# Performance work log

Hardware: AMD Instinct MI355X
Metric: run time of the kernel (lower is better)

Reference implementation:

```python
import jax, jax.numpy as jnp
from jax import lax
import numpy as np

N, E = 10000, 120000
IN_DIM = 128
HID = 32        # hidden_dim
HEADS = 8
OUT = 32        # out_dim
HD = HID * HEADS  # 256
EPS = 1e-5


def _bn(x, g, b):
    # BatchNorm1d (training-mode batch stats, deterministic reference)
    mu = x.mean(0)
    var = x.var(0)
    return g * (x - mu) * lax.rsqrt(var + EPS) + b


def _seg_softmax(logits, seg, n):
    # softmax over edges grouped by destination node, per head
    m = jax.ops.segment_max(logits, seg, num_segments=n)
    ex = jnp.exp(logits - m[seg])
    s = jax.ops.segment_sum(ex, seg, num_segments=n)
    return ex / (s[seg] + 1e-16)


def _gat_layer(h, src, dst, fc_w, a_l, a_r, bn_g, bn_b, heads, out, residual):
    n = h.shape[0]
    h_in = h
    feat = (h @ fc_w).reshape(n, heads, out)      # [N,H,D]
    el = (feat * a_l).sum(-1)                     # [N,H]
    er = (feat * a_r).sum(-1)
    logits = jax.nn.leaky_relu(el[src] + er[dst], 0.2)  # [E,H]
    alpha = _seg_softmax(logits, dst, n)
    rst = jax.ops.segment_sum(alpha[..., None] * feat[src], dst, num_segments=n)
    rst = rst.reshape(n, heads * out)
    rst = _bn(rst, bn_g, bn_b)
    rst = jax.nn.elu(rst)
    if residual:
        rst = h_in + rst
    return rst


def setup_inputs():
    key = jax.random.key(0)
    ks = jax.random.split(key, 20)
    s = 0.02
    d = {}
    d["h"] = jax.random.normal(ks[0], (N, IN_DIM), jnp.float32)
    d["e"] = jax.random.normal(ks[1], (E, IN_DIM), jnp.float32)
    d["src"] = jax.random.randint(ks[2], (E,), 0, N, jnp.int32)
    d["dst"] = jax.random.randint(ks[3], (E,), 0, N, jnp.int32)
    d["W_emb"] = jax.random.normal(ks[4], (IN_DIM, HD)) * s
    d["b_emb"] = jnp.zeros((HD,))
    d["W_p1"] = jax.random.normal(ks[5], (IN_DIM, HID * HID)) * s
    d["b_p1"] = jnp.zeros((HID * HID,))
    d["W_p2"] = jax.random.normal(ks[6], (IN_DIM, HID)) * s
    d["b_p2"] = jnp.zeros((HID,))
    d["W_conv"] = jax.random.normal(ks[7], (1, 2, 3)) * s  # Conv1d(2->1,k=3)
    d["b_conv"] = jnp.zeros((1,))
    d["W_ep2"] = jax.random.normal(ks[8], (IN_DIM, HD)) * s
    d["b_ep2"] = jnp.zeros((HD,))
    d["W_ep3"] = jax.random.normal(ks[9], (HID, HD)) * s
    d["b_ep3"] = jnp.zeros((HD,))
    d["bn_g"] = jnp.ones((HD,))
    d["bn_b"] = jnp.zeros((HD,))
    d["fc1"] = jax.random.normal(ks[10], (HD, HD)) * s
    d["al1"] = jax.random.normal(ks[11], (HEADS, HID)) * s
    d["ar1"] = jax.random.normal(ks[12], (HEADS, HID)) * s
    d["g1"] = jnp.ones((HD,))
    d["b1"] = jnp.zeros((HD,))
    d["fc2"] = jax.random.normal(ks[13], (HD, OUT)) * s
    d["al2"] = jax.random.normal(ks[14], (1, OUT)) * s
    d["ar2"] = jax.random.normal(ks[15], (1, OUT)) * s
    d["g2"] = jnp.ones((OUT,))
    d["b2"] = jnp.zeros((OUT,))
    return d


def reference(h, e, src, dst, W_emb, b_emb, W_p1, b_p1, W_p2, b_p2,
              W_conv, b_conv, W_ep2, b_ep2, W_ep3, b_ep3, bn_g, bn_b,
              fc1, al1, ar1, g1, b1, fc2, al2, ar2, g2, b2):
    # local edge feature: Conv1d over stacked (src,dst) node feats
    edge = jnp.stack([h[src], h[dst]], axis=1)  # [E,2,IN_DIM]
    conv = lax.conv_general_dilated(edge, W_conv, (1,), [(1, 1)],
                                    dimension_numbers=("NCH", "OIH", "NCH"))
    lr_local = conv[:, 0, :] + b_conv[0]         # [E,IN_DIM]
    lr_e_local = lr_local @ W_ep2 + b_ep2        # [E,HD]
    # low-rank global affinity: mm[i,j,k] = sum_d p1[i,k,d]*p2[j,d],
    # gathered only at edges (same math as the dense NxNxHID tensor)
    p1 = (h @ W_p1 + b_p1).reshape(-1, HID, HID)  # [N,HID,HID]
    p2 = h @ W_p2 + b_p2                          # [N,HID]
    lr_glob = jnp.einsum("ekd,ed->ek", p1[src], p2[dst])  # [E,HID]
    lr_e_global = lr_glob @ W_ep3 + b_ep3        # [E,HD]
    e_feat = jax.nn.relu(_bn(lr_e_local + lr_e_global, bn_g, bn_b))
    del e_feat  # default 'dgl' GATLayer ignores e; kept for faithfulness of math
    hh = h @ W_emb + b_emb                       # embedding_h
    hh = _gat_layer(hh, src, dst, fc1, al1, ar1, g1, b1, HEADS, HID, True)
    hh = _gat_layer(hh, src, dst, fc2, al2, ar2, g2, b2, 1, OUT, False)
    return hh
```

## Files before the change

### kernel.cpp

```cpp
#include <hip/hip_runtime.h>
#include <hip/hip_bf16.h>
#include <math.h>


#define HDIM 256
#define NHEADS 8
#define ODIM 32

typedef unsigned short u16;
typedef __attribute__((ext_vector_type(8))) short short8;
typedef __attribute__((ext_vector_type(4))) float f32x4;

__device__ __forceinline__ float bf2f(u16 u) { return __uint_as_float(((unsigned)u) << 16); }
__device__ __forceinline__ u16 f2bf(float f) {
    unsigned x = __float_as_uint(f);
    return (u16)((x + 0x7FFFu + ((x >> 16) & 1u)) >> 16);
}

__global__ __launch_bounds__(256) void prep_kernel(const float* __restrict__ in_h, const float* __restrict__ W_emb,
                                                   const float* __restrict__ fc1, const float* __restrict__ fc2,
                                                   u16* __restrict__ Ah, u16* __restrict__ Bemb,
                                                   u16* __restrict__ Bfc1, u16* __restrict__ Bfc2, int n4) {
    int job = blockIdx.y;
    int idx = blockIdx.x * 256 + threadIdx.x;
    if (job == 0) {
        if (idx >= n4) return;
        float4 v = ((const float4*)in_h)[idx];
        ushort4 o = {f2bf(v.x), f2bf(v.y), f2bf(v.z), f2bf(v.w)};
        ((ushort4*)Ah)[idx] = o;
        return;
    }
    const float* B;
    u16* O;
    int K, NC;
    if (job == 1) { B = W_emb; O = Bemb; K = 128; NC = 256; }
    else if (job == 2) { B = fc1; O = Bfc1; K = 256; NC = 256; }
    else { B = fc2; O = Bfc2; K = 256; NC = 32; }
    int KB = K / 32;
    int TOT = (NC / 16) * KB * 64;
    if (idx >= TOT) return;
    int lane = idx & 63;
    int kb = (idx >> 6) % KB;
    int ct = (idx >> 6) / KB;
    int n = ct * 16 + (lane & 15);
    int k0 = kb * 32 + (lane >> 4) * 8;
    u16* dst = O + (size_t)idx * 8;
#pragma unroll
    for (int j = 0; j < 8; j++) dst[j] = f2bf(B[(size_t)(k0 + j) * NC + n]);
}

__global__ __launch_bounds__(256) void deg_kernel(const int* __restrict__ dst, int* __restrict__ deg, int E, int N) {
    int i = blockIdx.x * 256 + threadIdx.x;
    if (i < E) {
        unsigned d = (unsigned)dst[i];
        if (d < (unsigned)N) atomicAdd(&deg[d], 1);
    }
}

__global__ __launch_bounds__(256) void scan_kernel(const int* __restrict__ deg, int* __restrict__ offs,
                                                   int* __restrict__ cursor, int n) {
    __shared__ int part[256];
    int t = threadIdx.x;
    int chunk = (n + 255) / 256;
    int lo = t * chunk, hi = lo + chunk;
    if (hi > n) hi = n;
    if (lo > n) lo = n;
    int s = 0;
    for (int i = lo; i < hi; i++) s += deg[i];
    part[t] = s;
    __syncthreads();
    if (t == 0) {
        int run = 0;
        for (int j = 0; j < 256; j++) { int v = part[j]; part[j] = run; run += v; }
        offs[n] = run;
    }
    __syncthreads();
    int run = part[t];
    for (int i = lo; i < hi; i++) {
        offs[i] = run;
        cursor[i] = run;
        run += deg[i];
    }
}

__global__ __launch_bounds__(256) void fill_kernel(const int* __restrict__ src, const int* __restrict__ dst,
                                                   int* __restrict__ cursor, int* __restrict__ srcs, int E, int N) {
    int i = blockIdx.x * 256 + threadIdx.x;
    if (i < E) {
        unsigned d = (unsigned)dst[i];
        if (d < (unsigned)N) {
            int p = atomicAdd(&cursor[d], 1);
            if ((unsigned)p < (unsigned)E) srcs[p] = src[i];
        }
    }
}

template <int K, int NC, bool BIAS, typename OutT>
__global__ __launch_bounds__(256) void gemm_mfma(const u16* __restrict__ A, const u16* __restrict__ Bsw,
                                                 const float* __restrict__ bias, OutT* __restrict__ C, int M) {
    constexpr int KB = K / 32;
    constexpr int NCT = NC / 16;
    const int lane = threadIdx.x & 63;
    const int r0 = blockIdx.x * 64 + (threadIdx.x >> 6) * 16;
    if (r0 >= M) return;
    const int m = lane & 15, q = lane >> 4;
    const int row = r0 + m;
    short8 a[KB];
#pragma unroll
    for (int kb = 0; kb < KB; kb++) {
        if (row < M) a[kb] = *(const short8*)(A + (size_t)row * K + kb * 32 + q * 8);
        else a[kb] = (short8){0, 0, 0, 0, 0, 0, 0, 0};
    }
    const short8* B8 = (const short8*)Bsw;
#pragma unroll 1
    for (int ct = 0; ct < NCT; ct++) {
        f32x4 acc = {0.f, 0.f, 0.f, 0.f};
#pragma unroll
        for (int kb = 0; kb < KB; kb++)
            acc = __builtin_amdgcn_mfma_f32_16x16x32_bf16(a[kb], B8[(ct * KB + kb) * 64 + lane], acc, 0, 0, 0);
        float bv = BIAS ? bias[ct * 16 + m] : 0.f;
#pragma unroll
        for (int r = 0; r < 4; r++) {
            int ro = r0 + q * 4 + r;
            if (ro < M) {
                float v = acc[r] + bv;
                if constexpr (sizeof(OutT) == 2) C[(size_t)ro * NC + ct * 16 + m] = f2bf(v);
                else C[(size_t)ro * NC + ct * 16 + m] = v;
            }
        }
    }
}

__global__ __launch_bounds__(256) void gemm_fc1_elr(const u16* __restrict__ A, const u16* __restrict__ Bsw,
                                                    const float* __restrict__ al, const float* __restrict__ ar,
                                                    u16* __restrict__ featC, u16* __restrict__ el,
                                                    u16* __restrict__ er, int M) {
    __shared__ u16 tile[64][256];
    const int lane = threadIdx.x & 63;
    const int wq = threadIdx.x >> 6;
    const int rb = blockIdx.x * 64;
    const int r0 = rb + wq * 16;
    const int m = lane & 15, q = lane >> 4;
    const int row = r0 + m;
    short8 a[8];
#pragma unroll
    for (int kb = 0; kb < 8; kb++) {
        if (row < M) a[kb] = *(const short8*)(A + (size_t)row * 256 + kb * 32 + q * 8);
        else a[kb] = (short8){0, 0, 0, 0, 0, 0, 0, 0};
    }
    const short8* B8 = (const short8*)Bsw;
#pragma unroll 1
    for (int ct = 0; ct < 16; ct++) {
        f32x4 acc = {0.f, 0.f, 0.f, 0.f};
#pragma unroll
        for (int kb = 0; kb < 8; kb++)
            acc = __builtin_amdgcn_mfma_f32_16x16x32_bf16(a[kb], B8[(ct * 8 + kb) * 64 + lane], acc, 0, 0, 0);
#pragma unroll
        for (int r = 0; r < 4; r++) {
            int rl = wq * 16 + q * 4 + r;
            int ro = rb + rl;
            u16 v = 0;
            if (ro < M) {
                v = f2bf(acc[r]);
                featC[(size_t)ro * 256 + ct * 16 + m] = v;
            }
            tile[rl][ct * 16 + m] = v;
        }
    }
    __syncthreads();
    int t = threadIdx.x;
#pragma unroll
    for (int task = t; task < 512; task += 256) {
        int nl = task >> 3, h = task & 7;
        int node = rb + nl;
        if (node >= M) continue;
        float a_ = 0.f, b_ = 0.f;
#pragma unroll
        for (int d = 0; d < 32; d++) {
            float fv = bf2f(tile[nl][h * 32 + d]);
            a_ += fv * al[h * 32 + d];
            b_ += fv * ar[h * 32 + d];
        }
        el[node * 8 + h] = f2bf(a_);
        er[node * 8 + h] = f2bf(b_);
    }
}

__device__ __forceinline__ float edgew(float l) {
    l = (l > 0.f) ? l : 0.2f * l;
    l = fminf(fmaxf(l, -30.f), 30.f);
    return __expf(l);
}

__global__ __launch_bounds__(256) void agg1_fused(const u16* __restrict__ feat, const u16* __restrict__ el,
                                                  const u16* __restrict__ er, const int* __restrict__ offs,
                                                  const int* __restrict__ srcs, u16* __restrict__ rst, int N, int E) {
    const int node = blockIdx.x * 4 + (threadIdx.x >> 6);
    const int lane = threadIdx.x & 63;
    if (node >= N) return;
    const int h = lane >> 3;
    int beg = offs[node], end = offs[node + 1];
    if (beg < 0) beg = 0;
    if (end > E) end = E;
    float ern = bf2f(er[node * 8 + h]);
    float ax = 0.f, ay = 0.f, az = 0.f, aw = 0.f, sw = 0.f;
    int j = beg;
    int end4 = beg + ((end - beg) & ~3);
    for (; j < end4; j += 4) {
        int s0 = srcs[j], s1 = srcs[j + 1], s2 = srcs[j + 2], s3 = srcs[j + 3];
        unsigned c0 = (unsigned)s0 < (unsigned)N, c1 = (unsigned)s1 < (unsigned)N;
        unsigned c2 = (unsigned)s2 < (unsigned)N, c3 = (unsigned)s3 < (unsigned)N;
        s0 = c0 ? s0 : 0; s1 = c1 ? s1 : 0; s2 = c2 ? s2 : 0; s3 = c3 ? s3 : 0;
        u16 e0 = el[s0 * 8 + h], e1 = el[s1 * 8 + h], e2 = el[s2 * 8 + h], e3 = el[s3 * 8 + h];
        ushort4 f0 = *(const ushort4*)(feat + (size_t)s0 * 256 + lane * 4);
        ushort4 f1 = *(const ushort4*)(feat + (size_t)s1 * 256 + lane * 4);
        ushort4 f2 = *(const ushort4*)(feat + (size_t)s2 * 256 + lane * 4);
        ushort4 f3 = *(const ushort4*)(feat + (size_t)s3 * 256 + lane * 4);
        float w0 = c0 ? edgew(bf2f(e0) + ern) : 0.f;
        float w1 = c1 ? edgew(bf2f(e1) + ern) : 0.f;
        float w2 = c2 ? edgew(bf2f(e2) + ern) : 0.f;
        float w3 = c3 ? edgew(bf2f(e3) + ern) : 0.f;
        sw += w0 + w1 + w2 + w3;
        ax += w0 * bf2f(f0.x) + w1 * bf2f(f1.x) + w2 * bf2f(f2.x) + w3 * bf2f(f3.x);
        ay += w0 * bf2f(f0.y) + w1 * bf2f(f1.y) + w2 * bf2f(f2.y) + w3 * bf2f(f3.y);
        az += w0 * bf2f(f0.z) + w1 * bf2f(f1.z) + w2 * bf2f(f2.z) + w3 * bf2f(f3.z);
        aw += w0 * bf2f(f0.w) + w1 * bf2f(f1.w) + w2 * bf2f(f2.w) + w3 * bf2f(f3.w);
    }
    for (; j < end; j++) {
        int s = srcs[j];
        if ((unsigned)s >= (unsigned)N) continue;
        float wv = edgew(bf2f(el[s * 8 + h]) + ern);
        ushort4 f4 = *(const ushort4*)(feat + (size_t)s * 256 + lane * 4);
        sw += wv;
        ax += wv * bf2f(f4.x);
        ay += wv * bf2f(f4.y);
        az += wv * bf2f(f4.z);
        aw += wv * bf2f(f4.w);
    }
    float inv = 1.f / (sw + 1e-16f);
    ushort4 o;
    o.x = f2bf(ax * inv); o.y = f2bf(ay * inv); o.z = f2bf(az * inv); o.w = f2bf(aw * inv);
    *(ushort4*)(rst + (size_t)node * 256 + lane * 4) = o;
}

__global__ __launch_bounds__(256) void bn_stats256(const u16* __restrict__ X, float* __restrict__ stats,
                                                   int rows, int RPB) {
    int t = threadIdx.x;
    int rbeg = blockIdx.x * RPB;
    int rend = rbeg + RPB;
    if (rend > rows) rend = rows;
    float s = 0.f, s2 = 0.f;
    for (int r = rbeg; r < rend; r++) {
        float x = bf2f(X[(long)r * 256 + t]);
        s += x;
        s2 += x * x;
    }
    atomicAdd(&stats[t], s);
    atomicAdd(&stats[256 + t], s2);
}

__global__ __launch_bounds__(256) void bn_stats32(const float* __restrict__ X, float* __restrict__ stats,
                                                  int rows, int RPB) {
    __shared__ float ss[256], ss2[256];
    int t = threadIdx.x, c = t & 31, rs = t >> 5;
    int rbeg = blockIdx.x * RPB;
    int rend = rbeg + RPB;
    if (rend > rows) rend = rows;
    float s = 0.f, s2 = 0.f;
    for (int r = rbeg + rs; r < rend; r += 8) {
        float x = X[(long)r * 32 + c];
        s += x;
        s2 += x * x;
    }
    ss[t] = s;
    ss2[t] = s2;
    __syncthreads();
    if (t < 32) {
        for (int j = 32; j < 256; j += 32) { s += ss[t + j]; s2 += ss2[t + j]; }
        atomicAdd(&stats[c], s);
        atomicAdd(&stats[32 + c], s2);
    }
}

__global__ __launch_bounds__(256) void gemm_fc2_fused(const u16* __restrict__ rst, const u16* __restrict__ hh,
                                                      const float* __restrict__ stats, const float* __restrict__ g,
                                                      const float* __restrict__ b, const u16* __restrict__ Bsw,
                                                      const float* __restrict__ al2, const float* __restrict__ ar2,
                                                      float* __restrict__ feat2, float* __restrict__ el2,
                                                      float* __restrict__ er2, int M, float invN) {
    __shared__ float sc[256], sh[256];
    __shared__ float tile[64][32];
    const int t = threadIdx.x;
    {
        float mu = stats[t] * invN;
        float var = fmaxf(stats[256 + t] * invN - mu * mu, 0.f);
        float s = g[t] * rsqrtf(var + 1e-5f);
        sc[t] = s;
        sh[t] = b[t] - mu * s;
    }
    __syncthreads();
    const int lane = t & 63, wq = t >> 6;
    const int rb = blockIdx.x * 64;
    const int m = lane & 15, q = lane >> 4;
    const int row = rb + wq * 16 + m;
    short8 a[8];
#pragma unroll
    for (int kb = 0; kb < 8; kb++) {
        if (row < M) {
            int k0 = kb * 32 + q * 8;
            ushort4 r01 = *(const ushort4*)(rst + (size_t)row * 256 + k0);
            ushort4 r23 = *(const ushort4*)(rst + (size_t)row * 256 + k0 + 4);
            ushort4 h01 = *(const ushort4*)(hh + (size_t)row * 256 + k0);
            ushort4 h23 = *(const ushort4*)(hh + (size_t)row * 256 + k0 + 4);
            u16 rv[8] = {r01.x, r01.y, r01.z, r01.w, r23.x, r23.y, r23.z, r23.w};
            u16 hv[8] = {h01.x, h01.y, h01.z, h01.w, h23.x, h23.y, h23.z, h23.w};
            short8 av;
#pragma unroll
            for (int j = 0; j < 8; j++) {
                int c = k0 + j;
                float y = sc[c] * bf2f(rv[j]) + sh[c];
                y = (y > 0.f) ? y : expm1f(y);
                av[j] = (short)f2bf(bf2f(hv[j]) + y);
            }
            a[kb] = av;
        } else a[kb] = (short8){0, 0, 0, 0, 0, 0, 0, 0};
    }
    const short8* B8 = (const short8*)Bsw;
#pragma unroll
    for (int ct = 0; ct < 2; ct++) {
        f32x4 acc = {0.f, 0.f, 0.f, 0.f};
#pragma unroll
        for (int kb = 0; kb < 8; kb++)
            acc = __builtin_amdgcn_mfma_f32_16x16x32_bf16(a[kb], B8[(ct * 8 + kb) * 64 + lane], acc, 0, 0, 0);
#pragma unroll
        for (int r = 0; r < 4; r++) {
            int rl = wq * 16 + q * 4 + r;
            int ro = rb + rl;
            float v = 0.f;
            if (ro < M) {
                v = acc[r];
                feat2[(size_t)ro * 32 + ct * 16 + m] = v;
            }
            tile[rl][ct * 16 + m] = v;
        }
    }
    __syncthreads();
    if (t < 64) {
        int node = rb + t;
        if (node < M) {
            float a_ = 0.f, b_ = 0.f;
#pragma unroll
            for (int d = 0; d < 32; d++) {
                float fv = tile[t][d];
                a_ += fv * al2[d];
                b_ += fv * ar2[d];
            }
            el2[node] = a_;
            er2[node] = b_;
        }
    }
}

__global__ __launch_bounds__(256) void agg2_fused(const float* __restrict__ feat, const float* __restrict__ el,
                                                  const float* __restrict__ er, const int* __restrict__ offs,
                                                  const int* __restrict__ srcs, float* __restrict__ rst,
                                                  int N, int E) {
    const int t = threadIdx.x;
    const int node = blockIdx.x * 8 + (t >> 5);
    const int d = t & 31;
    if (node >= N) return;
    int beg = offs[node], end = offs[node + 1];
    if (beg < 0) beg = 0;
    if (end > E) end = E;
    float ern = er[node];
    float acc = 0.f, sw = 0.f;
#pragma unroll 2
    for (int j = beg; j < end; j++) {
        int s = srcs[j];
        if ((unsigned)s >= (unsigned)N) continue;
        float wv = edgew(el[s] + ern);
        sw += wv;
        acc += wv * feat[(size_t)s * 32 + d];
    }
    rst[(size_t)node * 32 + d] = acc / (sw + 1e-16f);
}

__global__ __launch_bounds__(256) void bn_apply2(const float* __restrict__ rst, const float* __restrict__ stats,
                                                 const float* __restrict__ g, const float* __restrict__ b,
                                                 float* __restrict__ out, int total, float invN) {
    int idx = blockIdx.x * 256 + threadIdx.x;
    if (idx >= total) return;
    int c = idx & 31;
    float mu = stats[c] * invN;
    float var = fmaxf(stats[32 + c] * invN - mu * mu, 0.f);
    float y = g[c] * (rst[idx] - mu) * rsqrtf(var + 1e-5f) + b[c];
    y = (y > 0.f) ? y : expm1f(y);
    out[idx] = y;
}

extern "C" void kernel_launch(void* const* d_in, const int* in_sizes, int n_in, void* d_out, int out_size, void* d_ws,
                              size_t ws_size, hipStream_t stream) {
    const int N = out_size / ODIM;
    const int E = in_sizes[2];

    const int* src = (const int*)d_in[2];
    const int* dst = (const int*)d_in[3];
    const float* in_h = (const float*)d_in[0];
    const float* W_emb = (const float*)d_in[4];  const float* b_emb = (const float*)d_in[5];
    const float* fc1 = (const float*)d_in[18];   const float* al1 = (const float*)d_in[19];
    const float* ar1 = (const float*)d_in[20];
    const float* g1 = (const float*)d_in[21];    const float* b1 = (const float*)d_in[22];
    const float* fc2 = (const float*)d_in[23];   const float* al2 = (const float*)d_in[24];
    const float* ar2 = (const float*)d_in[25];
    const float* g2 = (const float*)d_in[26];    const float* b2 = (const float*)d_in[27];
    float* out = (float*)d_out;

    char* base = (char*)d_ws;
    size_t off = 0;
    auto alloc = [&](size_t bytes) { void* p = base + off; off += (bytes + 63) & ~63ull; return p; };
    char* zb   = (char*)alloc((size_t)N * 4 + 512 * 4 + 64 * 4);
    int* deg   = (int*)zb;
    float* stats  = (float*)(zb + (size_t)N * 4);
    float* stats2 = stats + 512;
    int* offs  = (int*)alloc((size_t)(N + 1) * 4);
    int* cursor = (int*)alloc((size_t)N * 4);
    int* srcs  = (int*)alloc((size_t)E * 4);
    u16* Ah    = (u16*)alloc((size_t)N * 128 * 2);
    u16* Bemb  = (u16*)alloc((size_t)128 * 256 * 2);
    u16* Bfc1  = (u16*)alloc((size_t)256 * 256 * 2);
    u16* Bfc2  = (u16*)alloc((size_t)256 * 32 * 2);
    u16* hh    = (u16*)alloc((size_t)N * HDIM * 2);
    u16* feat1 = (u16*)alloc((size_t)N * HDIM * 2);
    u16* el1   = (u16*)alloc((size_t)N * 8 * 2);
    u16* er1   = (u16*)alloc((size_t)N * 8 * 2);
    u16* rst   = (u16*)alloc((size_t)N * HDIM * 2);
    float* feat2 = (float*)alloc((size_t)N * 32 * 4);
    float* el2 = (float*)alloc((size_t)N * 4);
    float* er2 = (float*)alloc((size_t)N * 4);
    float* rst2 = (float*)alloc((size_t)N * 32 * 4);

    const int NB64 = (N + 63) / 64;

    hipMemsetAsync(zb, 0, (size_t)N * 4 + 512 * 4 + 64 * 4, stream);
    prep_kernel<<<dim3((N * 128 / 4 + 255) / 256, 4), 256, 0, stream>>>(in_h, W_emb, fc1, fc2, Ah, Bemb, Bfc1, Bfc2,
                                                                        N * 128 / 4);
    deg_kernel<<<(E + 255) / 256, 256, 0, stream>>>(dst, deg, E, N);
    scan_kernel<<<1, 256, 0, stream>>>(deg, offs, cursor, N);
    fill_kernel<<<(E + 255) / 256, 256, 0, stream>>>(src, dst, cursor, srcs, E, N);
    gemm_mfma<128, 256, true, u16><<<NB64, 256, 0, stream>>>(Ah, Bemb, b_emb, hh, N);
    gemm_fc1_elr<<<NB64, 256, 0, stream>>>(hh, Bfc1, al1, ar1, feat1, el1, er1, N);
    agg1_fused<<<(N + 3) / 4, 256, 0, stream>>>(feat1, el1, er1, offs, srcs, rst, N, E);
    bn_stats256<<<(N + 39) / 40, 256, 0, stream>>>(rst, stats, N, 40);
    gemm_fc2_fused<<<NB64, 256, 0, stream>>>(rst, hh, stats, g1, b1, Bfc2, al2, ar2, feat2, el2, er2, N, 1.f / N);
    agg2_fused<<<(N + 7) / 8, 256, 0, stream>>>(feat2, el2, er2, offs, srcs, rst2, N, E);
    bn_stats32<<<(N + 63) / 64, 256, 0, stream>>>(rst2, stats2, N, 64);
    bn_apply2<<<(N * ODIM + 255) / 256, 256, 0, stream>>>(rst2, stats2, g2, b2, out, N * ODIM, 1.f / N);
}
```

Baseline: 286.1 us.

## Fuse embedding and fc1 GEMMs, merge degree/fill into other kernels, warp-scan

Folds the degree-count atomics into the prep kernel as an extra job, and merges the CSR fill with the fused embedding+fc1 GEMM kernel through extra blocks. Inside that kernel the embedding output stays in an XOR-swizzled LDS tile and feeds the fc1 MFMA directly. The scan kernel's serial single-thread prefix is replaced with a wavefront shuffle scan. Together these cut three kernel launches, a global round trip of hh into fc1, and serial scan work. The cost is heterogeneous blocks in one grid and more LDS traffic per block.

```diff
diff --git a/kernel.cpp b/kernel.cpp
--- a/kernel.cpp
+++ b/kernel.cpp
@@ -19,8 +19,10 @@
 
 __global__ __launch_bounds__(256) void prep_kernel(const float* __restrict__ in_h, const float* __restrict__ W_emb,
                                                    const float* __restrict__ fc1, const float* __restrict__ fc2,
+                                                   const int* __restrict__ dstv, int* __restrict__ deg,
                                                    u16* __restrict__ Ah, u16* __restrict__ Bemb,
-                                                   u16* __restrict__ Bfc1, u16* __restrict__ Bfc2, int n4) {
+                                                   u16* __restrict__ Bfc1, u16* __restrict__ Bfc2,
+                                                   int n4, int E, int N) {
     int job = blockIdx.y;
     int idx = blockIdx.x * 256 + threadIdx.x;
     if (job == 0) {
@@ -28,6 +30,13 @@
         float4 v = ((const float4*)in_h)[idx];
         ushort4 o = {f2bf(v.x), f2bf(v.y), f2bf(v.z), f2bf(v.w)};
         ((ushort4*)Ah)[idx] = o;
+        return;
+    }
+    if (job == 4) {
+        if (idx < E) {
+            unsigned d = (unsigned)dstv[idx];
+            if (d < (unsigned)N) atomicAdd(&deg[d], 1);
+        }
         return;
     }
     const float* B;
@@ -49,17 +58,9 @@
     for (int j = 0; j < 8; j++) dst[j] = f2bf(B[(size_t)(k0 + j) * NC + n]);
 }
 
-__global__ __launch_bounds__(256) void deg_kernel(const int* __restrict__ dst, int* __restrict__ deg, int E, int N) {
-    int i = blockIdx.x * 256 + threadIdx.x;
-    if (i < E) {
-        unsigned d = (unsigned)dst[i];
-        if (d < (unsigned)N) atomicAdd(&deg[d], 1);
-    }
-}
-
 __global__ __launch_bounds__(256) void scan_kernel(const int* __restrict__ deg, int* __restrict__ offs,
                                                    int* __restrict__ cursor, int n) {
-    __shared__ int part[256];
+    __shared__ int wsum[4];
     int t = threadIdx.x;
     int chunk = (n + 255) / 256;
     int lo = t * chunk, hi = lo + chunk;
@@ -67,94 +68,100 @@
     if (lo > n) lo = n;
     int s = 0;
     for (int i = lo; i < hi; i++) s += deg[i];
-    part[t] = s;
-    __syncthreads();
-    if (t == 0) {
-        int run = 0;
-        for (int j = 0; j < 256; j++) { int v = part[j]; part[j] = run; run += v; }
-        offs[n] = run;
-    }
-    __syncthreads();
-    int run = part[t];
+    int v = s;
+#pragma unroll
+    for (int d = 1; d < 64; d <<= 1) {
+        int nb = __shfl_up(v, d, 64);
+        if ((t & 63) >= d) v += nb;
+    }
+    if ((t & 63) == 63) wsum[t >> 6] = v;
+    __syncthreads();
+    int woff = 0;
+#pragma unroll
+    for (int w = 0; w < 4; w++)
+        if (w < (t >> 6)) woff += wsum[w];
+    int run = woff + v - s;
     for (int i = lo; i < hi; i++) {
         offs[i] = run;
         cursor[i] = run;
         run += deg[i];
     }
-}
-
-__global__ __launch_bounds__(256) void fill_kernel(const int* __restrict__ src, const int* __restrict__ dst,
-                                                   int* __restrict__ cursor, int* __restrict__ srcs, int E, int N) {
-    int i = blockIdx.x * 256 + threadIdx.x;
-    if (i < E) {
-        unsigned d = (unsigned)dst[i];
-        if (d < (unsigned)N) {
-            int p = atomicAdd(&cursor[d], 1);
-            if ((unsigned)p < (unsigned)E) srcs[p] = src[i];
-        }
-    }
-}
-
-template <int K, int NC, bool BIAS, typename OutT>
-__global__ __launch_bounds__(256) void gemm_mfma(const u16* __restrict__ A, const u16* __restrict__ Bsw,
-                                                 const float* __restrict__ bias, OutT* __restrict__ C, int M) {
-    constexpr int KB = K / 32;
-    constexpr int NCT = NC / 16;
-    const int lane = threadIdx.x & 63;
-    const int r0 = blockIdx.x * 64 + (threadIdx.x >> 6) * 16;
-    if (r0 >= M) return;
+    if (t == 255) offs[n] = run;
+}
+
+__global__ __launch_bounds__(256) void fused_emb_fc1(const u16* __restrict__ Ah, const u16* __restrict__ Bemb,
+                                                     const float* __restrict__ bemb, const u16* __restrict__ Bfc1,
+                                                     const float* __restrict__ al, const float* __restrict__ ar,
+                                                     u16* __restrict__ hh, u16* __restrict__ feat1,
+                                                     u16* __restrict__ el, u16* __restrict__ er,
+                                                     const int* __restrict__ src, const int* __restrict__ dstv,
+                                                     int* __restrict__ cursor, int* __restrict__ srcs,
+                                                     int M, int NB, int E, int N) {
+    if ((int)blockIdx.x >= NB) {
+        int i = ((int)blockIdx.x - NB) * 256 + (int)threadIdx.x;
+        if (i < E) {
+            unsigned d = (unsigned)dstv[i];
+            if (d < (unsigned)N) {
+                int p = atomicAdd(&cursor[d], 1);
+                if ((unsigned)p < (unsigned)E) srcs[p] = src[i];
+            }
+        }
+        return;
+    }
+    __shared__ u16 tile[64 * 256];
+    const int t = threadIdx.x;
+    const int lane = t & 63, wq = t >> 6;
+    const int rb = (int)blockIdx.x * 64;
     const int m = lane & 15, q = lane >> 4;
-    const int row = r0 + m;
-    short8 a[KB];
-#pragma unroll
-    for (int kb = 0; kb < KB; kb++) {
-        if (row < M) a[kb] = *(const short8*)(A + (size_t)row * K + kb * 32 + q * 8);
-        else a[kb] = (short8){0, 0, 0, 0, 0, 0, 0, 0};
-    }
-    const short8* B8 = (const short8*)Bsw;
-#pragma unroll 1
-    for (int ct = 0; ct < NCT; ct++) {
-        f32x4 acc = {0.f, 0.f, 0.f, 0.f};
-#pragma unroll
-        for (int kb = 0; kb < KB; kb++)
-            acc = __builtin_amdgcn_mfma_f32_16x16x32_bf16(a[kb], B8[(ct * KB + kb) * 64 + lane], acc, 0, 0, 0);
-        float bv = BIAS ? bias[ct * 16 + m] : 0.f;
-#pragma unroll
-        for (int r = 0; r < 4; r++) {
-            int ro = r0 + q * 4 + r;
-            if (ro < M) {
-                float v = acc[r] + bv;
-                if constexpr (sizeof(OutT) == 2) C[(size_t)ro * NC + ct * 16 + m] = f2bf(v);
-                else C[(size_t)ro * NC + ct * 16 + m] = v;
-            }
-        }
-    }
-}
-
-__global__ __launch_bounds__(256) void gemm_fc1_elr(const u16* __restrict__ A, const u16* __restrict__ Bsw,
-                                                    const float* __restrict__ al, const float* __restrict__ ar,
-                                                    u16* __restrict__ featC, u16* __restrict__ el,
-                                                    u16* __restrict__ er, int M) {
-    __shared__ u16 tile[64][256];
-    const int lane = threadIdx.x & 63;
-    const int wq = threadIdx.x >> 6;
-    const int rb = blockIdx.x * 64;
-    const int r0 = rb + wq * 16;
-    const int m = lane & 15, q = lane >> 4;
-    const int row = r0 + m;
-    short8 a[8];
-#pragma unroll
-    for (int kb = 0; kb < 8; kb++) {
-        if (row < M) a[kb] = *(const short8*)(A + (size_t)row * 256 + kb * 32 + q * 8);
-        else a[kb] = (short8){0, 0, 0, 0, 0, 0, 0, 0};
-    }
-    const short8* B8 = (const short8*)Bsw;
+    const int row = rb + wq * 16 + m;
+
+    short8 a0[4];
+#pragma unroll
+    for (int kb = 0; kb < 4; kb++) {
+        if (row < M) a0[kb] = *(const short8*)(Ah + (size_t)row * 128 + kb * 32 + q * 8);
+        else a0[kb] = (short8){0, 0, 0, 0, 0, 0, 0, 0};
+    }
+    const short8* B8 = (const short8*)Bemb;
 #pragma unroll 1
     for (int ct = 0; ct < 16; ct++) {
         f32x4 acc = {0.f, 0.f, 0.f, 0.f};
 #pragma unroll
+        for (int kb = 0; kb < 4; kb++)
+            acc = __builtin_amdgcn_mfma_f32_16x16x32_bf16(a0[kb], B8[(ct * 4 + kb) * 64 + lane], acc, 0, 0, 0);
+        float bv = bemb[ct * 16 + m];
+#pragma unroll
+        for (int r = 0; r < 4; r++) {
+            int rl = wq * 16 + q * 4 + r;
+            int ro = rb + rl;
+            u16 hv = 0;
+            if (ro < M) {
+                hv = f2bf(acc[r] + bv);
+                hh[(size_t)ro * 256 + ct * 16 + m] = hv;
+            }
+            int byte = rl * 512 + (ct * 16 + m) * 2;
+            tile[(byte ^ ((rl & 7) << 4)) >> 1] = hv;
+        }
+    }
+    __syncthreads();
+
+    short8 af[8];
+    {
+        int rl = wq * 16 + m;
+#pragma unroll
+        for (int kb = 0; kb < 8; kb++) {
+            int byte = rl * 512 + kb * 64 + q * 16;
+            af[kb] = *(const short8*)(tile + ((byte ^ ((rl & 7) << 4)) >> 1));
+        }
+    }
+    __syncthreads();
+
+    const short8* Bf = (const short8*)Bfc1;
+#pragma unroll 1
+    for (int ct = 0; ct < 16; ct++) {
+        f32x4 acc = {0.f, 0.f, 0.f, 0.f};
+#pragma unroll
         for (int kb = 0; kb < 8; kb++)
-            acc = __builtin_amdgcn_mfma_f32_16x16x32_bf16(a[kb], B8[(ct * 8 + kb) * 64 + lane], acc, 0, 0, 0);
+            acc = __builtin_amdgcn_mfma_f32_16x16x32_bf16(af[kb], Bf[(ct * 8 + kb) * 64 + lane], acc, 0, 0, 0);
 #pragma unroll
         for (int r = 0; r < 4; r++) {
             int rl = wq * 16 + q * 4 + r;
@@ -162,27 +169,27 @@
             u16 v = 0;
             if (ro < M) {
                 v = f2bf(acc[r]);
-                featC[(size_t)ro * 256 + ct * 16 + m] = v;
-            }
-            tile[rl][ct * 16 + m] = v;
-        }
-    }
-    __syncthreads();
-    int t = threadIdx.x;
+                feat1[(size_t)ro * 256 + ct * 16 + m] = v;
+            }
+            tile[rl * 256 + ct * 16 + m] = v;
+        }
+    }
+    __syncthreads();
+
 #pragma unroll
     for (int task = t; task < 512; task += 256) {
-        int nl = task >> 3, h = task & 7;
+        int nl = task >> 3, h2 = task & 7;
         int node = rb + nl;
         if (node >= M) continue;
         float a_ = 0.f, b_ = 0.f;
 #pragma unroll
         for (int d = 0; d < 32; d++) {
-            float fv = bf2f(tile[nl][h * 32 + d]);
-            a_ += fv * al[h * 32 + d];
-            b_ += fv * ar[h * 32 + d];
-        }
-        el[node * 8 + h] = f2bf(a_);
-        er[node * 8 + h] = f2bf(b_);
+            float fv = bf2f(tile[nl * 256 + h2 * 32 + d]);
+            a_ += fv * al[h2 * 32 + d];
+            b_ += fv * ar[h2 * 32 + d];
+        }
+        el[node * 8 + h2] = f2bf(a_);
+        er[node * 8 + h2] = f2bf(b_);
     }
 }
 
@@ -440,15 +447,14 @@
     float* rst2 = (float*)alloc((size_t)N * 32 * 4);
 
     const int NB64 = (N + 63) / 64;
+    const int NBF = (E + 255) / 256;
 
     hipMemsetAsync(zb, 0, (size_t)N * 4 + 512 * 4 + 64 * 4, stream);
-    prep_kernel<<<dim3((N * 128 / 4 + 255) / 256, 4), 256, 0, stream>>>(in_h, W_emb, fc1, fc2, Ah, Bemb, Bfc1, Bfc2,
-                                                                        N * 128 / 4);
-    deg_kernel<<<(E + 255) / 256, 256, 0, stream>>>(dst, deg, E, N);
+    prep_kernel<<<dim3((N * 128 / 4 + 255) / 256, 5), 256, 0, stream>>>(in_h, W_emb, fc1, fc2, dst, deg,
+                                                                        Ah, Bemb, Bfc1, Bfc2, N * 128 / 4, E, N);
     scan_kernel<<<1, 256, 0, stream>>>(deg, offs, cursor, N);
-    fill_kernel<<<(E + 255) / 256, 256, 0, stream>>>(src, dst, cursor, srcs, E, N);
-    gemm_mfma<128, 256, true, u16><<<NB64, 256, 0, stream>>>(Ah, Bemb, b_emb, hh, N);
-    gemm_fc1_elr<<<NB64, 256, 0, stream>>>(hh, Bfc1, al1, ar1, feat1, el1, er1, N);
+    fused_emb_fc1<<<NB64 + NBF, 256, 0, stream>>>(Ah, Bemb, b_emb, Bfc1, al1, ar1, hh, feat1, el1, er1,
+                                                  src, dst, cursor, srcs, N, NB64, E, N);
     agg1_fused<<<(N + 3) / 4, 256, 0, stream>>>(feat1, el1, er1, offs, srcs, rst, N, E);
     bn_stats256<<<(N + 39) / 40, 256, 0, stream>>>(rst, stats, N, 40);
     gemm_fc2_fused<<<NB64, 256, 0, stream>>>(rst, hh, stats, g1, b1, Bfc2, al2, ar2, feat2, el2, er2, N, 1.f / N);
```

After: 276.5 us. -3.3%, faster.
